# Optimization experiments

Hardware: AMD Instinct MI355X
Metric: run time of the kernel (lower is better)

## Reference

```python
import jax, jax.numpy as jnp
import numpy as np

B, C, H, W, NH = 8, 256, 32, 32, 4  # batch, channels, height, width, heads


def groupnorm(x, w, b, eps=1e-5):
    # GroupNorm with 1 group: normalize over (C,H,W) per sample
    mu = x.mean(axis=(1, 2, 3), keepdims=True)
    var = x.var(axis=(1, 2, 3), keepdims=True)
    xn = (x - mu) * jax.lax.rsqrt(var + eps)
    return xn * w[None, :, None, None] + b[None, :, None, None]


def setup_inputs() -> dict:
    key = jax.random.key(0)
    ks = jax.random.split(key, 6)
    C4 = 4 * C
    s = lambda k, shape, scale: jax.random.normal(k, shape, jnp.float32) * scale
    return {
        "x": jax.random.normal(ks[0], (B, C, H, W), jnp.float32),
        "qkv_w": s(ks[1], (3 * C, C), 0.05),   # 1x1 conv, no bias
        "uh_w": s(ks[2], (C, C), 0.05),
        "uh_b": jnp.zeros((C,), jnp.float32),
        "n1_w": jnp.ones((C,), jnp.float32),
        "n1_b": jnp.zeros((C,), jnp.float32),
        "n2_w": jnp.ones((C,), jnp.float32),
        "n2_b": jnp.zeros((C,), jnp.float32),
        "f1_w": s(ks[3], (C4, C), 0.05),
        "f1_b": jnp.zeros((C4,), jnp.float32),
        "f2_w": s(ks[4], (C, C4), 0.05),
        "f2_b": jnp.zeros((C,), jnp.float32),
        # torch inits these to 0; use nonzero values so both branches contribute
        "gamma_attn": jnp.array(0.5, jnp.float32),
        "gamma_ffn": jnp.array(0.5, jnp.float32),
    }


def reference(x, qkv_w, uh_w, uh_b, n1_w, n1_b, n2_w, n2_b,
              f1_w, f1_b, f2_w, f2_b, gamma_attn, gamma_ffn):
    Bx, Cx, Hx, Wx = x.shape
    N = Hx * Wx
    dk = Cx // NH
    # --- attention branch (eval mode: DropPath is identity) ---
    xn = groupnorm(x, n1_w, n1_b).reshape(Bx, Cx, N)
    qkv = jnp.einsum('oc,bcn->bon', qkv_w, xn)          # 1x1 conv == channel matmul
    q, k, v = [t.reshape(Bx, NH, dk, N) for t in jnp.split(qkv, 3, axis=1)]
    scores = jnp.einsum('bhdi,bhdj->bhij', q, k) / np.float32(np.sqrt(dk))
    attn = jax.nn.softmax(scores, axis=-1)               # [B,H,N,N]
    out = jnp.einsum('bhij,bhdj->bhdi', attn, v).reshape(Bx, Cx, N)
    uh = jnp.einsum('oc,bcn->bon', uh_w, out) + uh_b[None, :, None]
    x2 = x + gamma_attn * uh.reshape(Bx, Cx, Hx, Wx)
    # --- FFN branch ---
    h = groupnorm(x2, n2_w, n2_b).reshape(Bx, Cx, N)
    h = jax.nn.silu(jnp.einsum('oc,bcn->bon', f1_w, h) + f1_b[None, :, None])
    h = jnp.einsum('oc,bcn->bon', f2_w, h) + f2_b[None, :, None]
    return x2 + gamma_ffn * h.reshape(Bx, Cx, Hx, Wx)
```

## Files before the change

kernel.cpp:

```cpp
#include <hip/hip_runtime.h>
#include <math.h>

#define Bsz 8
#define Cch 256
#define Nsp 1024
#define NHd 4
#define QS  0.18033688011112042f

using bf16x8  = __attribute__((ext_vector_type(8))) short;
using f32x4   = __attribute__((ext_vector_type(4))) float;
using ushort8 = __attribute__((ext_vector_type(8))) unsigned short;
#define MFMA(a,b,c) __builtin_amdgcn_mfma_f32_16x16x32_bf16(a,b,c,0,0,0)

__device__ inline unsigned short f2bf(float f) {
    unsigned int u = __float_as_uint(f);
    u = u + 0x7fffu + ((u >> 16) & 1u);
    return (unsigned short)(u >> 16);
}
__device__ inline float bf2f(unsigned short u) {
    return __uint_as_float((unsigned int)u << 16);
}
__device__ inline unsigned int cvtpk(float lo, float hi) {
    unsigned int r;
    asm("v_cvt_pk_bf16_f32 %0, %1, %2" : "=v"(r) : "v"(lo), "v"(hi));
    return r;
}

__global__ __launch_bounds__(256) void wconv_gn(const float* __restrict__ a, const float* __restrict__ b,
                                                const float* __restrict__ c, const float* __restrict__ d,
                                                unsigned short* __restrict__ o,
                                                const float* __restrict__ x,
                                                float* __restrict__ part) {
    if (blockIdx.x < 3072) {
        size_t i = (size_t)blockIdx.x * 256 + threadIdx.x;
        float v;
        if (i < 196608) v = a[i];
        else if (i < 262144) v = b[i - 196608];
        else if (i < 524288) v = c[i - 262144];
        else v = d[i - 524288];
        o[i] = f2bf(v);
        return;
    }
    int blk = blockIdx.x - 3072;
    int bb = blk >> 6;
    const float* xb = x + (size_t)bb * (Cch * Nsp) + (size_t)(blk & 63) * 4096;
    int t = threadIdx.x;
    float s = 0.f, s2 = 0.f;
    for (int i = t; i < 4096; i += 256) { float v = xb[i]; s += v; s2 += v * v; }
    __shared__ float sh[256], sh2[256];
    sh[t] = s; sh2[t] = s2; __syncthreads();
    for (int off = 128; off; off >>= 1) {
        if (t < off) { sh[t] += sh[t + off]; sh2[t] += sh2[t + off]; }
        __syncthreads();
    }
    if (t == 0) { part[blk * 2] = sh[0]; part[blk * 2 + 1] = sh2[0]; }
}

__global__ __launch_bounds__(256) void gn_apply_t(const float* __restrict__ x,
                                                  const float* __restrict__ part, int npart,
                                                  const float* __restrict__ w,
                                                  const float* __restrict__ bb,
                                                  unsigned short* __restrict__ out_cl) {
    int b = blockIdx.z, c0 = blockIdx.y * 64, n0 = blockIdx.x * 64;
    __shared__ float tile[64][65];
    __shared__ float smu, srs;
    int t = threadIdx.x;
    if (t < 64) {
        float s = 0.f, s2 = 0.f;
        for (int u = t; u < npart; u += 64) {
            s += part[(b * npart + u) * 2]; s2 += part[(b * npart + u) * 2 + 1];
        }
        for (int m = 1; m < 64; m <<= 1) { s += __shfl_xor(s, m); s2 += __shfl_xor(s2, m); }
        if (t == 0) {
            float inv_n = 1.f / (Cch * Nsp);
            float mu = s * inv_n;
            float var = s2 * inv_n - mu * mu;
            smu = mu; srs = rsqrtf(var + 1e-5f);
        }
    }
    const float* xb = x + ((size_t)b * Cch + c0) * Nsp + n0;
    for (int i = 0; i < 16; i++) {
        int e = t + i * 256; int r = e >> 6, c = e & 63;
        tile[r][c] = xb[(size_t)r * Nsp + c];
    }
    __syncthreads();
    float mu = smu, rs = srs;
    unsigned short* ob = out_cl + ((size_t)b * Nsp + n0) * Cch + c0;
    for (int i = 0; i < 16; i++) {
        int e = t + i * 256; int nr = e >> 6, nc = e & 63;
        int c = c0 + nc;
        float v = (tile[nc][nr] - mu) * rs * w[c] + bb[c];
        ob[(size_t)nr * Cch + nc] = f2bf(v);
    }
}

template<int K, int KL, int NFRAG>
__global__ __launch_bounds__(256, (K > 256) ? 2 : 4) void gemm_lds(
        const unsigned short* __restrict__ W,
        const unsigned short* __restrict__ Xcl,
        int epi, int act, int xmode,
        unsigned short* __restrict__ ocl, int Ocl, int ocol0,
        unsigned short* __restrict__ orm,
        float* __restrict__ pf, const float* __restrict__ res,
        unsigned short* __restrict__ x2cl,
        const float* __restrict__ gamma, const float* __restrict__ bias,
        float* __restrict__ part,
        const float* __restrict__ gnpart,
        const float* __restrict__ gnw, const float* __restrict__ gnb) {
    static_assert(KL == 256, "K-loop hardcoded for KL=256 (8 steps)");
    constexpr int NK = K / KL;
    constexpr int NTILE = NFRAG * 16;
    constexpr int CPR = KL / 8;
    constexpr int TOTCH = NTILE * CPR;
    int b = blockIdx.z, nb = blockIdx.x, ob = blockIdx.y;
    int t = threadIdx.x, w = t >> 6, l = t & 63, lg = l >> 4, lm = l & 15;
    __shared__ unsigned short Xs[(NK > 1 ? 2 : 1) * NTILE * KL];
    __shared__ float sgn[2];
    unsigned short* Xs0 = Xs;
    unsigned short* Xs1 = Xs + (NK > 1 ? NTILE * KL : 0);
    const unsigned short* Xb = Xcl + ((size_t)b * Nsp + nb * NTILE) * K;
    int o_base = ob * 256 + w * 64;
    const unsigned short* Wp = W + (size_t)(o_base + lm) * K + 8 * lg;
    int m8 = lm & 7;

    bf16x8 wr[3][4];
    #define WLOAD(sl, g_) do {                                             \
        const unsigned short* wp_ = Wp + ((g_) >> 3) * KL + ((g_) & 7) * 32; \
        wr[sl][0] = *(const bf16x8*)(wp_);                                 \
        wr[sl][1] = *(const bf16x8*)(wp_ + (size_t)16 * K);                \
        wr[sl][2] = *(const bf16x8*)(wp_ + (size_t)32 * K);                \
        wr[sl][3] = *(const bf16x8*)(wp_ + (size_t)48 * K);                \
    } while (0)
    WLOAD(0, 0);
    WLOAD(1, 1);

    if (xmode == 0) {
        #pragma unroll
        for (int i = 0; i < TOTCH / 256; i++) {
            int c = i * 256 + t;
            int n = c / CPR, s = c % CPR;
            int gc = s ^ (n & 7);
            *(bf16x8*)&Xs0[c * 8] = *(const bf16x8*)(Xb + (size_t)n * K + gc * 8);
        }
    } else if (xmode == 1) {
        if (t < 64) {
            float s = gnpart[(b * 64 + t) * 2], s2 = gnpart[(b * 64 + t) * 2 + 1];
            for (int m = 1; m < 64; m <<= 1) { s += __shfl_xor(s, m); s2 += __shfl_xor(s2, m); }
            if (t == 0) {
                float inv_n = 1.f / (Cch * Nsp);
                float mu = s * inv_n;
                float var = s2 * inv_n - mu * mu;
                sgn[0] = mu; sgn[1] = rsqrtf(var + 1e-5f);
            }
        }
        __syncthreads();
        float mu = sgn[0], rs = sgn[1];
        #pragma unroll
        for (int i = 0; i < TOTCH / 256; i++) {
            int c = i * 256 + t;
            int n = c / CPR, s = c % CPR;
            int gc = s ^ (n & 7);
            ushort8 xv = *(const ushort8*)(Xb + (size_t)n * K + gc * 8);
            f32x4 w0 = *(const f32x4*)(gnw + gc * 8);
            f32x4 w1 = *(const f32x4*)(gnw + gc * 8 + 4);
            f32x4 b0 = *(const f32x4*)(gnb + gc * 8);
            f32x4 b1 = *(const f32x4*)(gnb + gc * 8 + 4);
            ushort8 rr;
            #pragma unroll
            for (int j = 0; j < 4; j++) {
                rr[j]     = f2bf((bf2f(xv[j])     - mu) * rs * w0[j] + b0[j]);
                rr[4 + j] = f2bf((bf2f(xv[4 + j]) - mu) * rs * w1[j] + b1[j]);
            }
            *(ushort8*)&Xs0[c * 8] = rr;
        }
    } else {
        const size_t SPO = (size_t)Bsz * Nsp * Cch;
        #pragma unroll
        for (int i = 0; i < TOTCH / 256; i++) {
            int c = i * 256 + t;
            int n = c / CPR, s = c % CPR;
            int gc = s ^ (n & 7);
            const unsigned short* p0 = Xb + (size_t)n * K + gc * 8;
            int h = gc >> 3;
            int gn = nb * NTILE + n;
            float a0[8] = {};
            float lsum = 0.f;
            #pragma unroll
            for (int sp = 0; sp < 4; sp++) {
                ushort8 ov = *(const ushort8*)(p0 + (size_t)sp * SPO);
                #pragma unroll
                for (int j = 0; j < 8; j++) a0[j] += bf2f(ov[j]);
                lsum += gnpart[(((size_t)sp * Bsz + b) * NHd + h) * Nsp + gn];
            }
            float inv = 1.f / lsum;
            ushort8 rr;
            #pragma unroll
            for (int j = 0; j < 8; j++) rr[j] = f2bf(a0[j] * inv);
            *(ushort8*)&Xs0[c * 8] = rr;
        }
    }
    __syncthreads();

    f32x4 acc[4][NFRAG] = {};
    bf16x8 st[TOTCH / 256];
    #define KSTEP(sl, s_, Xp) do {                                         \
        _Pragma("unroll")                                                  \
        for (int nf = 0; nf < NFRAG; nf++) {                               \
            int slot = ((s_) * 4 + lg) ^ m8;                               \
            bf16x8 xf = *(const bf16x8*)&(Xp)[((nf * 16 + lm) * CPR + slot) * 8]; \
            acc[0][nf] = MFMA(wr[sl][0], xf, acc[0][nf]);                  \
            acc[1][nf] = MFMA(wr[sl][1], xf, acc[1][nf]);                  \
            acc[2][nf] = MFMA(wr[sl][2], xf, acc[2][nf]);                  \
            acc[3][nf] = MFMA(wr[sl][3], xf, acc[3][nf]);                  \
        }                                                                  \
    } while (0)

    #pragma unroll
    for (int g = 0; g < 8 * NK; g++) {
        const int r = g >> 3, s = g & 7;
        if (NK > 1 && r + 1 < NK && s == 0) {
            #pragma unroll
            for (int i = 0; i < TOTCH / 256; i++) {
                int c = i * 256 + t;
                int n = c / CPR, sc = c % CPR;
                int gc = sc ^ (n & 7);
                st[i] = *(const bf16x8*)(Xb + (size_t)n * K + (r + 1) * KL + gc * 8);
            }
        }
        if (g + 2 < 8 * NK) WLOAD((g + 2) % 3, g + 2);
        {
            const unsigned short* Xp = (r & 1) ? Xs1 : Xs0;
            KSTEP(g % 3, s, Xp);
        }
        if (NK > 1 && r + 1 < NK && s == 6) {
            unsigned short* dst = (r & 1) ? Xs0 : Xs1;
            #pragma unroll
            for (int i = 0; i < TOTCH / 256; i++) {
                int c = i * 256 + t;
                *(bf16x8*)&dst[c * 8] = st[i];
            }
        }
        if (NK > 1 && r + 1 < NK && s == 7) __syncthreads();
    }
    #undef WLOAD
    #undef KSTEP

    if (epi == 0) {
        if (act == 3 && o_base >= 512) {
            #pragma unroll
            for (int nf = 0; nf < NFRAG; nf++) {
                int n = nb * NTILE + nf * 16 + lm;
                #pragma unroll
                for (int q = 0; q < 4; q++)
                    #pragma unroll
                    for (int r = 0; r < 4; r++) {
                        int o = o_base + q * 16 + 4 * lg + r - 512;
                        orm[((size_t)b * Cch + o) * Nsp + n] = f2bf(acc[q][nf][r]);
                    }
            }
        } else {
            float sc = (act == 3 && o_base < 256) ? QS : 1.f;
            #pragma unroll
            for (int nf = 0; nf < NFRAG; nf++) {
                int n = nb * NTILE + nf * 16 + lm;
                unsigned short* dst = ocl + ((size_t)b * Nsp + n) * Ocl + ocol0 + o_base + 4 * lg;
                #pragma unroll
                for (int q = 0; q < 4; q++) {
                    unsigned long long pk = 0;
                    #pragma unroll
                    for (int r = 0; r < 4; r++) {
                        int o = o_base + q * 16 + 4 * lg + r;
                        float v = acc[q][nf][r];
                        if (bias) v += bias[o];
                        if (act == 1) v = v / (1.f + __expf(-v));
                        else v *= sc;
                        pk |= (unsigned long long)f2bf(v) << (16 * r);
                    }
                    *(unsigned long long*)(dst + q * 16) = pk;
                }
            }
        }
    } else if (epi == 2) {
        float g = gamma[0];
        float ps = 0.f, ps2 = 0.f;
        #pragma unroll
        for (int nf = 0; nf < NFRAG; nf++) {
            int n = nb * NTILE + nf * 16 + lm;
            unsigned short* cdst = x2cl + ((size_t)b * Nsp + n) * Cch + o_base + 4 * lg;
            #pragma unroll
            for (int q = 0; q < 4; q++) {
                unsigned long long pk = 0;
                #pragma unroll
                for (int r = 0; r < 4; r++) {
                    int o = o_base + q * 16 + 4 * lg + r;
                    float v = acc[q][nf][r];
                    if (bias) v += bias[o];
                    size_t idx = ((size_t)b * Cch + o) * Nsp + n;
                    float ov = res[idx] + g * v;
                    pf[idx] = ov;
                    ps += ov; ps2 += ov * ov;
                    pk |= (unsigned long long)f2bf(ov) << (16 * r);
                }
                *(unsigned long long*)(cdst + q * 16) = pk;
            }
        }
        float* rsh  = (float*)&Xs[0];
        float* rsh2 = rsh + 256;
        __syncthreads();
        rsh[t] = ps; rsh2[t] = ps2; __syncthreads();
        for (int off = 128; off; off >>= 1) {
            if (t < off) { rsh[t] += rsh[t + off]; rsh2[t] += rsh2[t + off]; }
            __syncthreads();
        }
        if (t == 0) {
            int slot = b * gridDim.x + nb;
            part[slot * 2] = rsh[0]; part[slot * 2 + 1] = rsh2[0];
        }
    } else {
        float g = gamma[0];
        #pragma unroll
        for (int nf = 0; nf < NFRAG; nf++) {
            int n = nb * NTILE + nf * 16 + lm;
            #pragma unroll
            for (int q = 0; q < 4; q++) {
                #pragma unroll
                for (int r = 0; r < 4; r++) {
                    int o = o_base + q * 16 + 4 * lg + r;
                    size_t idx = ((size_t)b * Cch + o) * Nsp + n;
                    pf[idx] = res[idx] + g * (acc[q][nf][r] + bias[o]);
                }
            }
        }
    }
}

__global__ __launch_bounds__(256) void attn_mfma8(const unsigned short* __restrict__ qk,
                                                  const unsigned short* __restrict__ v,
                                                  unsigned short* __restrict__ Opart,
                                                  float* __restrict__ lpart) {
    int L = blockIdx.x;
    int xcd = L & 7, jj = L >> 3;
    int g = xcd * 4 + (jj >> 5);
    int m = jj & 31;
    int h = g & 3, b = g >> 2;
    int ib = m & 7, sp = m >> 3;
    int t = threadIdx.x, w = t >> 6, l = t & 63, lg = l >> 4, lm = l & 15;
    __shared__ unsigned short KVs[2][4096];
    __shared__ unsigned short P[4][2][32][36];
    int i0 = ib * 128 + w * 32;
    int j0 = sp * 256;
    const unsigned short* qb = qk + ((size_t)b * Nsp + i0 + lm) * 512 + h * 64 + 8 * lg;
    bf16x8 qf00 = *(const bf16x8*)(qb);
    bf16x8 qf01 = *(const bf16x8*)(qb + 32);
    bf16x8 qf10 = *(const bf16x8*)(qb + 16 * 512);
    bf16x8 qf11 = *(const bf16x8*)(qb + 16 * 512 + 32);

    const unsigned short *gs0, *gs1;
    int lo0, lo1;
    size_t gstep;
    if (t < 128) {
        int c = 2 * t;
        int r = c >> 3, s = c & 7, swr = r & 7;
        const unsigned short* rowp = qk + ((size_t)b * Nsp + j0 + r) * 512 + 256 + h * 64;
        gs0 = rowp + ((s ^ swr) * 8);
        gs1 = rowp + (((s + 1) ^ swr) * 8);
        lo0 = c * 8; lo1 = lo0 + 8;
        gstep = (size_t)32 * 512;
    } else {
        int c = 2 * (t - 128);
        int d = c >> 2, s = c & 3, swd = d & 3;
        const unsigned short* rowp = v + ((size_t)b * Cch + h * 64 + d) * Nsp + j0;
        gs0 = rowp + ((s ^ swd) * 8);
        gs1 = rowp + (((s + 1) ^ swd) * 8);
        lo0 = 2048 + c * 8; lo1 = lo0 + 8;
        gstep = 32;
    }
    int cA = (lg ^ (lm & 7)) * 8;
    int cB = ((4 + lg) ^ (lm & 7)) * 8;
    int cV = (lg ^ (lm & 3)) * 8;

    f32x4 O00 = {}, O01 = {}, O02 = {}, O03 = {};
    f32x4 O10 = {}, O11 = {}, O12 = {}, O13 = {};
    float ls0 = 0.f, ls1 = 0.f;
    bf16x8 sg0, sg1;

    #define ISSUE(tile) do { sg0 = *(const bf16x8*)(gs0 + (size_t)(tile) * gstep); \
                             sg1 = *(const bf16x8*)(gs1 + (size_t)(tile) * gstep); } while (0)
    #define WRITE(bu) do { *(bf16x8*)&KVs[bu][lo0] = sg0; \
                           *(bf16x8*)&KVs[bu][lo1] = sg1; } while (0)
    #define QKC8(bu, pb) do {                                                     \
        const unsigned short* Ka = KVs[bu] + lm * 64;                             \
        const unsigned short* Kc = KVs[bu] + (16 + lm) * 64;                      \
        bf16x8 k00 = *(const bf16x8*)(Ka + cA);                                   \
        bf16x8 k01 = *(const bf16x8*)(Ka + cB);                                   \
        bf16x8 k10 = *(const bf16x8*)(Kc + cA);                                   \
        bf16x8 k11 = *(const bf16x8*)(Kc + cB);                                   \
        f32x4 s00 = {}, s01 = {}, s10 = {}, s11 = {};                             \
        s00 = MFMA(k00, qf00, s00); s00 = MFMA(k01, qf01, s00);                   \
        s01 = MFMA(k00, qf10, s01); s01 = MFMA(k01, qf11, s01);                   \
        s10 = MFMA(k10, qf00, s10); s10 = MFMA(k11, qf01, s10);                   \
        s11 = MFMA(k10, qf10, s11); s11 = MFMA(k11, qf11, s11);                   \
        float p0, p1, p2, p3; uint2 pk;                                           \
        p0 = exp2f(s00[0]); p1 = exp2f(s00[1]); p2 = exp2f(s00[2]); p3 = exp2f(s00[3]); \
        ls0 += (p0 + p1) + (p2 + p3);                                             \
        pk.x = cvtpk(p0, p1); pk.y = cvtpk(p2, p3);                               \
        *(uint2*)&P[w][pb][lm][4 * lg] = pk;                                      \
        p0 = exp2f(s01[0]); p1 = exp2f(s01[1]); p2 = exp2f(s01[2]); p3 = exp2f(s01[3]); \
        ls1 += (p0 + p1) + (p2 + p3);                                             \
        pk.x = cvtpk(p0, p1); pk.y = cvtpk(p2, p3);                               \
        *(uint2*)&P[w][pb][16 + lm][4 * lg] = pk;                                 \
        p0 = exp2f(s10[0]); p1 = exp2f(s10[1]); p2 = exp2f(s10[2]); p3 = exp2f(s10[3]); \
        ls0 += (p0 + p1) + (p2 + p3);                                             \
        pk.x = cvtpk(p0, p1); pk.y = cvtpk(p2, p3);                               \
        *(uint2*)&P[w][pb][lm][16 + 4 * lg] = pk;                                 \
        p0 = exp2f(s11[0]); p1 = exp2f(s11[1]); p2 = exp2f(s11[2]); p3 = exp2f(s11[3]); \
        ls1 += (p0 + p1) + (p2 + p3);                                             \
        pk.x = cvtpk(p0, p1); pk.y = cvtpk(p2, p3);                               \
        *(uint2*)&P[w][pb][16 + lm][16 + 4 * lg] = pk;                            \
    } while (0)
    #define PVC8(bu, pb) do {                                                     \
        bf16x8 pa0 = *(const bf16x8*)&P[w][pb][lm][8 * lg];                       \
        bf16x8 pa1 = *(const bf16x8*)&P[w][pb][16 + lm][8 * lg];                  \
        const unsigned short* Vl = KVs[bu] + 2048;                                \
        bf16x8 v0 = *(const bf16x8*)(Vl + lm * 32 + cV);                          \
        bf16x8 v1 = *(const bf16x8*)(Vl + (16 + lm) * 32 + cV);                   \
        bf16x8 v2 = *(const bf16x8*)(Vl + (32 + lm) * 32 + cV);                   \
        bf16x8 v3 = *(const bf16x8*)(Vl + (48 + lm) * 32 + cV);                   \
        O00 = MFMA(v0, pa0, O00); O10 = MFMA(v0, pa1, O10);                       \
        O01 = MFMA(v1, pa0, O01); O11 = MFMA(v1, pa1, O11);                       \
        O02 = MFMA(v2, pa0, O02); O12 = MFMA(v2, pa1, O12);                       \
        O03 = MFMA(v3, pa0, O03); O13 = MFMA(v3, pa1, O13);                       \
    } while (0)

    ISSUE(0); WRITE(0); __syncthreads();
    ISSUE(1);
    QKC8(0, 0);
    __syncthreads();
    WRITE(1);
    __syncthreads();
    #pragma unroll
    for (int tt = 1; tt < 8; tt++) {
        if (tt < 7) ISSUE(tt + 1);
        QKC8(tt & 1, tt & 1);
        PVC8((tt - 1) & 1, (tt - 1) & 1);
        __syncthreads();
        if (tt < 7) WRITE((tt + 1) & 1);
        __syncthreads();
    }
    PVC8(1, 1);
    #undef ISSUE
    #undef WRITE
    #undef QKC8
    #undef PVC8

    ls0 += __shfl_xor(ls0, 16); ls0 += __shfl_xor(ls0, 32);
    ls1 += __shfl_xor(ls1, 16); ls1 += __shfl_xor(ls1, 32);
    if (lg == 0) {
        float* lp = lpart + (((size_t)sp * Bsz + b) * NHd + h) * Nsp + i0 + lm;
        lp[0] = ls0;
        lp[16] = ls1;
    }
    unsigned short* ob0 = Opart + (((size_t)sp * Bsz + b) * Nsp + i0 + lm) * Cch + h * 64 + 4 * lg;
    unsigned short* ob1 = ob0 + (size_t)16 * Cch;
    uint2 pk;
    #define STO(dt, Oa, Ob_) \
        pk.x = cvtpk(Oa[0], Oa[1]); pk.y = cvtpk(Oa[2], Oa[3]); \
        *(uint2*)(ob0 + dt * 16) = pk; \
        pk.x = cvtpk(Ob_[0], Ob_[1]); pk.y = cvtpk(Ob_[2], Ob_[3]); \
        *(uint2*)(ob1 + dt * 16) = pk;
    STO(0, O00, O10) STO(1, O01, O11) STO(2, O02, O12) STO(3, O03, O13)
    #undef STO
}

extern "C" void kernel_launch(void* const* d_in, const int* in_sizes, int n_in,
                              void* d_out, int out_size, void* d_ws, size_t ws_size,
                              hipStream_t stream) {
    const float* x      = (const float*)d_in[0];
    const float* qkv_w  = (const float*)d_in[1];
    const float* uh_w   = (const float*)d_in[2];
    const float* uh_b   = (const float*)d_in[3];
    const float* n1_w   = (const float*)d_in[4];
    const float* n1_b   = (const float*)d_in[5];
    const float* n2_w   = (const float*)d_in[6];
    const float* n2_b   = (const float*)d_in[7];
    const float* f1_w   = (const float*)d_in[8];
    const float* f1_b   = (const float*)d_in[9];
    const float* f2_w   = (const float*)d_in[10];
    const float* f2_b   = (const float*)d_in[11];
    const float* g_attn = (const float*)d_in[12];
    const float* g_ffn  = (const float*)d_in[13];
    float* out = (float*)d_out;
    char* ws = (char*)d_ws;

    float*          part1   = (float*)(ws + 1024);
    float*          part2   = (float*)(ws + 5120);
    unsigned short* wbf     = (unsigned short*)(ws + 16384);
    unsigned short* xn_cl   = (unsigned short*)(ws + 2097152);
    float*          lpart   = (float*)(ws + 2097152);
    unsigned short* qk_cl   = (unsigned short*)(ws + 6291456);
    unsigned short* vbuf    = (unsigned short*)(ws + 14680064);
    unsigned short* x2cl    = (unsigned short*)(ws + 14680064);
    unsigned short* Opart   = (unsigned short*)(ws + 23068672);
    unsigned short* h1_cl   = (unsigned short*)(ws + 31457280);
    float*          x2      = (float*)(ws + 50331648);

    unsigned short* wbf_qkv = wbf;
    unsigned short* wbf_uh  = wbf + 196608;
    unsigned short* wbf_f1  = wbf + 262144;
    unsigned short* wbf_f2  = wbf + 524288;

    wconv_gn<<<3584, 256, 0, stream>>>(qkv_w, uh_w, f1_w, f2_w, wbf, x, part1);

    gn_apply_t<<<dim3(16, 4, Bsz), 256, 0, stream>>>(x, part1, 64, n1_w, n1_b, xn_cl);
    gemm_lds<256, 256, 2><<<dim3(32, 3, Bsz), 256, 0, stream>>>(wbf_qkv, xn_cl, 0, 3, 0,
        qk_cl, 512, 0, vbuf, nullptr, nullptr, nullptr, nullptr, nullptr, nullptr,
        nullptr, nullptr, nullptr);
    attn_mfma8<<<1024, 256, 0, stream>>>(qk_cl, vbuf, Opart, lpart);
    gemm_lds<256, 256, 1><<<dim3(64, 1, Bsz), 256, 0, stream>>>(wbf_uh, Opart, 2, 0, 2,
        nullptr, 0, 0, nullptr, x2, x, x2cl, g_attn, uh_b, part2,
        lpart, nullptr, nullptr);

    gemm_lds<256, 256, 2><<<dim3(32, 4, Bsz), 256, 0, stream>>>(wbf_f1, x2cl, 0, 1, 1,
        h1_cl, 1024, 0, nullptr, nullptr, nullptr, nullptr, nullptr, f1_b, nullptr,
        part2, n2_w, n2_b);
    gemm_lds<1024, 256, 2><<<dim3(32, 1, Bsz), 256, 0, stream>>>(wbf_f2, h1_cl, 5, 0, 0,
        nullptr, 0, 0, nullptr, out, x2, nullptr, g_ffn, f2_b, nullptr,
        nullptr, nullptr, nullptr);
}
```

Before: 118.4 us.

## Fuse GroupNorm-1 into QKV GEMM and fuse both FFN GEMMs into one kernel

Drops the separate gn_apply_t transpose kernel. The QKV GEMM now reads fp32 x directly, normalizes it and stores it channel-last into LDS (new xmode 3). The FFN1 and FFN2 GEMMs are merged into a single ffn_fused kernel that keeps the 32x1024 SiLU hidden tile in LDS, so the h1 round trip through global memory and two launches are removed. The trade-off is 80KB of LDS per block in ffn_fused, which limits occupancy, and only 256 blocks for that stage. The generic GEMM drops its multi-round K path.

```diff
diff --git a/kernel.cpp b/kernel.cpp
--- a/kernel.cpp
+++ b/kernel.cpp
@@ -56,46 +56,8 @@
     if (t == 0) { part[blk * 2] = sh[0]; part[blk * 2 + 1] = sh2[0]; }
 }
 
-__global__ __launch_bounds__(256) void gn_apply_t(const float* __restrict__ x,
-                                                  const float* __restrict__ part, int npart,
-                                                  const float* __restrict__ w,
-                                                  const float* __restrict__ bb,
-                                                  unsigned short* __restrict__ out_cl) {
-    int b = blockIdx.z, c0 = blockIdx.y * 64, n0 = blockIdx.x * 64;
-    __shared__ float tile[64][65];
-    __shared__ float smu, srs;
-    int t = threadIdx.x;
-    if (t < 64) {
-        float s = 0.f, s2 = 0.f;
-        for (int u = t; u < npart; u += 64) {
-            s += part[(b * npart + u) * 2]; s2 += part[(b * npart + u) * 2 + 1];
-        }
-        for (int m = 1; m < 64; m <<= 1) { s += __shfl_xor(s, m); s2 += __shfl_xor(s2, m); }
-        if (t == 0) {
-            float inv_n = 1.f / (Cch * Nsp);
-            float mu = s * inv_n;
-            float var = s2 * inv_n - mu * mu;
-            smu = mu; srs = rsqrtf(var + 1e-5f);
-        }
-    }
-    const float* xb = x + ((size_t)b * Cch + c0) * Nsp + n0;
-    for (int i = 0; i < 16; i++) {
-        int e = t + i * 256; int r = e >> 6, c = e & 63;
-        tile[r][c] = xb[(size_t)r * Nsp + c];
-    }
-    __syncthreads();
-    float mu = smu, rs = srs;
-    unsigned short* ob = out_cl + ((size_t)b * Nsp + n0) * Cch + c0;
-    for (int i = 0; i < 16; i++) {
-        int e = t + i * 256; int nr = e >> 6, nc = e & 63;
-        int c = c0 + nc;
-        float v = (tile[nc][nr] - mu) * rs * w[c] + bb[c];
-        ob[(size_t)nr * Cch + nc] = f2bf(v);
-    }
-}
-
 template<int K, int KL, int NFRAG>
-__global__ __launch_bounds__(256, (K > 256) ? 2 : 4) void gemm_lds(
+__global__ __launch_bounds__(256, 4) void gemm_lds(
         const unsigned short* __restrict__ W,
         const unsigned short* __restrict__ Xcl,
         int epi, int act, int xmode,
@@ -107,25 +69,22 @@
         float* __restrict__ part,
         const float* __restrict__ gnpart,
         const float* __restrict__ gnw, const float* __restrict__ gnb) {
-    static_assert(KL == 256, "K-loop hardcoded for KL=256 (8 steps)");
-    constexpr int NK = K / KL;
+    static_assert(KL == 256 && K == 256, "single-round K only");
     constexpr int NTILE = NFRAG * 16;
     constexpr int CPR = KL / 8;
     constexpr int TOTCH = NTILE * CPR;
     int b = blockIdx.z, nb = blockIdx.x, ob = blockIdx.y;
     int t = threadIdx.x, w = t >> 6, l = t & 63, lg = l >> 4, lm = l & 15;
-    __shared__ unsigned short Xs[(NK > 1 ? 2 : 1) * NTILE * KL];
+    __shared__ unsigned short Xs[NTILE * KL];
     __shared__ float sgn[2];
-    unsigned short* Xs0 = Xs;
-    unsigned short* Xs1 = Xs + (NK > 1 ? NTILE * KL : 0);
     const unsigned short* Xb = Xcl + ((size_t)b * Nsp + nb * NTILE) * K;
     int o_base = ob * 256 + w * 64;
     const unsigned short* Wp = W + (size_t)(o_base + lm) * K + 8 * lg;
-    int m8 = lm & 7;
+    int m8 = lm & 15 & 7;
 
     bf16x8 wr[3][4];
     #define WLOAD(sl, g_) do {                                             \
-        const unsigned short* wp_ = Wp + ((g_) >> 3) * KL + ((g_) & 7) * 32; \
+        const unsigned short* wp_ = Wp + ((g_) & 7) * 32;                  \
         wr[sl][0] = *(const bf16x8*)(wp_);                                 \
         wr[sl][1] = *(const bf16x8*)(wp_ + (size_t)16 * K);                \
         wr[sl][2] = *(const bf16x8*)(wp_ + (size_t)32 * K);                \
@@ -140,7 +99,7 @@
             int c = i * 256 + t;
             int n = c / CPR, s = c % CPR;
             int gc = s ^ (n & 7);
-            *(bf16x8*)&Xs0[c * 8] = *(const bf16x8*)(Xb + (size_t)n * K + gc * 8);
+            *(bf16x8*)&Xs[c * 8] = *(const bf16x8*)(Xb + (size_t)n * K + gc * 8);
         }
     } else if (xmode == 1) {
         if (t < 64) {
@@ -171,9 +130,9 @@
                 rr[j]     = f2bf((bf2f(xv[j])     - mu) * rs * w0[j] + b0[j]);
                 rr[4 + j] = f2bf((bf2f(xv[4 + j]) - mu) * rs * w1[j] + b1[j]);
             }
-            *(ushort8*)&Xs0[c * 8] = rr;
-        }
-    } else {
+            *(ushort8*)&Xs[c * 8] = rr;
+        }
+    } else if (xmode == 2) {
         const size_t SPO = (size_t)Bsz * Nsp * Cch;
         #pragma unroll
         for (int i = 0; i < TOTCH / 256; i++) {
@@ -196,51 +155,54 @@
             ushort8 rr;
             #pragma unroll
             for (int j = 0; j < 8; j++) rr[j] = f2bf(a0[j] * inv);
-            *(ushort8*)&Xs0[c * 8] = rr;
+            *(ushort8*)&Xs[c * 8] = rr;
+        }
+    } else {
+        if (t < 64) {
+            float s = gnpart[(b * 64 + t) * 2], s2 = gnpart[(b * 64 + t) * 2 + 1];
+            for (int m = 1; m < 64; m <<= 1) { s += __shfl_xor(s, m); s2 += __shfl_xor(s2, m); }
+            if (t == 0) {
+                float inv_n = 1.f / (Cch * Nsp);
+                float mu = s * inv_n;
+                float var = s2 * inv_n - mu * mu;
+                sgn[0] = mu; sgn[1] = rsqrtf(var + 1e-5f);
+            }
+        }
+        __syncthreads();
+        float mu = sgn[0], rs = sgn[1];
+        int n = t & 31;
+        #pragma unroll
+        for (int i = 0; i < 4; i++) {
+            int G = i * 8 + (t >> 5);
+            const float* xr = res + ((size_t)b * Cch + G * 8) * Nsp + (size_t)nb * NTILE + n;
+            ushort8 rr;
+            #pragma unroll
+            for (int j = 0; j < 8; j++) {
+                float val = xr[(size_t)j * Nsp];
+                rr[j] = f2bf((val - mu) * rs * gnw[G * 8 + j] + gnb[G * 8 + j]);
+            }
+            int slot = G ^ (n & 7);
+            *(ushort8*)&Xs[(n * 32 + slot) * 8] = rr;
         }
     }
     __syncthreads();
 
     f32x4 acc[4][NFRAG] = {};
-    bf16x8 st[TOTCH / 256];
-    #define KSTEP(sl, s_, Xp) do {                                         \
+    #define KSTEP(sl, s_) do {                                             \
         _Pragma("unroll")                                                  \
         for (int nf = 0; nf < NFRAG; nf++) {                               \
             int slot = ((s_) * 4 + lg) ^ m8;                               \
-            bf16x8 xf = *(const bf16x8*)&(Xp)[((nf * 16 + lm) * CPR + slot) * 8]; \
+            bf16x8 xf = *(const bf16x8*)&Xs[((nf * 16 + lm) * CPR + slot) * 8]; \
             acc[0][nf] = MFMA(wr[sl][0], xf, acc[0][nf]);                  \
             acc[1][nf] = MFMA(wr[sl][1], xf, acc[1][nf]);                  \
             acc[2][nf] = MFMA(wr[sl][2], xf, acc[2][nf]);                  \
             acc[3][nf] = MFMA(wr[sl][3], xf, acc[3][nf]);                  \
         }                                                                  \
     } while (0)
-
     #pragma unroll
-    for (int g = 0; g < 8 * NK; g++) {
-        const int r = g >> 3, s = g & 7;
-        if (NK > 1 && r + 1 < NK && s == 0) {
-            #pragma unroll
-            for (int i = 0; i < TOTCH / 256; i++) {
-                int c = i * 256 + t;
-                int n = c / CPR, sc = c % CPR;
-                int gc = sc ^ (n & 7);
-                st[i] = *(const bf16x8*)(Xb + (size_t)n * K + (r + 1) * KL + gc * 8);
-            }
-        }
-        if (g + 2 < 8 * NK) WLOAD((g + 2) % 3, g + 2);
-        {
-            const unsigned short* Xp = (r & 1) ? Xs1 : Xs0;
-            KSTEP(g % 3, s, Xp);
-        }
-        if (NK > 1 && r + 1 < NK && s == 6) {
-            unsigned short* dst = (r & 1) ? Xs0 : Xs1;
-            #pragma unroll
-            for (int i = 0; i < TOTCH / 256; i++) {
-                int c = i * 256 + t;
-                *(bf16x8*)&dst[c * 8] = st[i];
-            }
-        }
-        if (NK > 1 && r + 1 < NK && s == 7) __syncthreads();
+    for (int s = 0; s < 8; s++) {
+        if (s < 6) WLOAD((s + 2) % 3, s + 2);
+        KSTEP(s % 3, s);
     }
     #undef WLOAD
     #undef KSTEP
@@ -280,7 +242,7 @@
                 }
             }
         }
-    } else if (epi == 2) {
+    } else {
         float g = gamma[0];
         float ps = 0.f, ps2 = 0.f;
         #pragma unroll
@@ -316,19 +278,150 @@
             int slot = b * gridDim.x + nb;
             part[slot * 2] = rsh[0]; part[slot * 2 + 1] = rsh2[0];
         }
-    } else {
-        float g = gamma[0];
-        #pragma unroll
-        for (int nf = 0; nf < NFRAG; nf++) {
-            int n = nb * NTILE + nf * 16 + lm;
-            #pragma unroll
-            for (int q = 0; q < 4; q++) {
-                #pragma unroll
-                for (int r = 0; r < 4; r++) {
-                    int o = o_base + q * 16 + 4 * lg + r;
-                    size_t idx = ((size_t)b * Cch + o) * Nsp + n;
-                    pf[idx] = res[idx] + g * (acc[q][nf][r] + bias[o]);
-                }
+    }
+}
+
+__global__ __launch_bounds__(256, 2) void ffn_fused(
+        const unsigned short* __restrict__ Wf1,
+        const unsigned short* __restrict__ Wf2,
+        const unsigned short* __restrict__ x2cl,
+        const float* __restrict__ gnpart,
+        const float* __restrict__ gnw, const float* __restrict__ gnb,
+        const float* __restrict__ f1b, const float* __restrict__ f2b,
+        const float* __restrict__ gamma,
+        const float* __restrict__ x2, float* __restrict__ out) {
+    int b = blockIdx.z, nb = blockIdx.x;
+    int t = threadIdx.x, w = t >> 6, l = t & 63, lg = l >> 4, lm = l & 15;
+    __shared__ unsigned short Xs[32 * 256];
+    __shared__ unsigned short H[4][32 * 256];
+    __shared__ float sgn[2];
+    const unsigned short* Xb = x2cl + ((size_t)b * Nsp + nb * 32) * 256;
+    int m8 = lm & 7;
+
+    bf16x8 wr[3][4];
+    const unsigned short* Wp;
+    #define WLOADF(sl, g_, KK) do {                                        \
+        const unsigned short* wp_ = Wp + ((g_) >> 3) * 256 + ((g_) & 7) * 32; \
+        wr[sl][0] = *(const bf16x8*)(wp_);                                 \
+        wr[sl][1] = *(const bf16x8*)(wp_ + (size_t)16 * (KK));             \
+        wr[sl][2] = *(const bf16x8*)(wp_ + (size_t)32 * (KK));             \
+        wr[sl][3] = *(const bf16x8*)(wp_ + (size_t)48 * (KK));             \
+    } while (0)
+
+    if (t < 64) {
+        float s = gnpart[(b * 64 + t) * 2], s2 = gnpart[(b * 64 + t) * 2 + 1];
+        for (int m = 1; m < 64; m <<= 1) { s += __shfl_xor(s, m); s2 += __shfl_xor(s2, m); }
+        if (t == 0) {
+            float inv_n = 1.f / (Cch * Nsp);
+            float mu = s * inv_n;
+            float var = s2 * inv_n - mu * mu;
+            sgn[0] = mu; sgn[1] = rsqrtf(var + 1e-5f);
+        }
+    }
+    Wp = Wf1 + (size_t)(w * 64 + lm) * 256 + 8 * lg;
+    WLOADF(0, 0, 256);
+    WLOADF(1, 1, 256);
+    __syncthreads();
+    {
+        float mu = sgn[0], rs = sgn[1];
+        #pragma unroll
+        for (int i = 0; i < 4; i++) {
+            int c = i * 256 + t;
+            int n = c / 32, s = c % 32;
+            int gc = s ^ (n & 7);
+            ushort8 xv = *(const ushort8*)(Xb + (size_t)n * 256 + gc * 8);
+            f32x4 w0 = *(const f32x4*)(gnw + gc * 8);
+            f32x4 w1 = *(const f32x4*)(gnw + gc * 8 + 4);
+            f32x4 b0 = *(const f32x4*)(gnb + gc * 8);
+            f32x4 b1 = *(const f32x4*)(gnb + gc * 8 + 4);
+            ushort8 rr;
+            #pragma unroll
+            for (int j = 0; j < 4; j++) {
+                rr[j]     = f2bf((bf2f(xv[j])     - mu) * rs * w0[j] + b0[j]);
+                rr[4 + j] = f2bf((bf2f(xv[4 + j]) - mu) * rs * w1[j] + b1[j]);
+            }
+            *(ushort8*)&Xs[c * 8] = rr;
+        }
+    }
+    __syncthreads();
+
+    f32x4 acc[4][2];
+    #define KSTEPF(sl, s_, Xp) do {                                        \
+        _Pragma("unroll")                                                  \
+        for (int nf = 0; nf < 2; nf++) {                                   \
+            int slot = ((s_) * 4 + lg) ^ m8;                               \
+            bf16x8 xf = *(const bf16x8*)&(Xp)[((nf * 16 + lm) * 32 + slot) * 8]; \
+            acc[0][nf] = MFMA(wr[sl][0], xf, acc[0][nf]);                  \
+            acc[1][nf] = MFMA(wr[sl][1], xf, acc[1][nf]);                  \
+            acc[2][nf] = MFMA(wr[sl][2], xf, acc[2][nf]);                  \
+            acc[3][nf] = MFMA(wr[sl][3], xf, acc[3][nf]);                  \
+        }                                                                  \
+    } while (0)
+    #define F1PASS(obp, NEXTPROLOG) do {                                   \
+        _Pragma("unroll")                                                  \
+        for (int q = 0; q < 4; q++)                                        \
+            _Pragma("unroll")                                              \
+            for (int nf = 0; nf < 2; nf++) acc[q][nf] = (f32x4){0.f, 0.f, 0.f, 0.f}; \
+        _Pragma("unroll")                                                  \
+        for (int s = 0; s < 8; s++) {                                      \
+            if (s < 6) WLOADF((s + 2) % 3, s + 2, 256);                    \
+            KSTEPF(s % 3, s, Xs);                                          \
+        }                                                                  \
+        NEXTPROLOG;                                                        \
+        _Pragma("unroll")                                                  \
+        for (int nf = 0; nf < 2; nf++) {                                   \
+            int n = nf * 16 + lm;                                          \
+            _Pragma("unroll")                                              \
+            for (int q = 0; q < 4; q++) {                                  \
+                unsigned long long pk = 0;                                 \
+                _Pragma("unroll")                                          \
+                for (int r = 0; r < 4; r++) {                              \
+                    int oin = w * 64 + q * 16 + 4 * lg + r;                \
+                    float v = acc[q][nf][r] + f1b[(obp) * 256 + oin];      \
+                    v = v / (1.f + __expf(-v));                            \
+                    pk |= (unsigned long long)f2bf(v) << (16 * r);         \
+                }                                                          \
+                int G = w * 8 + q * 2 + (lg >> 1);                         \
+                int slot = G ^ (n & 7);                                    \
+                *(unsigned long long*)&H[obp][(n * 32 + slot) * 8 + 4 * (lg & 1)] = pk; \
+            }                                                              \
+        }                                                                  \
+    } while (0)
+
+    F1PASS(0, { Wp = Wf1 + (size_t)(256 + w * 64 + lm) * 256 + 8 * lg;
+                WLOADF(0, 0, 256); WLOADF(1, 1, 256); });
+    F1PASS(1, { Wp = Wf1 + (size_t)(512 + w * 64 + lm) * 256 + 8 * lg;
+                WLOADF(0, 0, 256); WLOADF(1, 1, 256); });
+    F1PASS(2, { Wp = Wf1 + (size_t)(768 + w * 64 + lm) * 256 + 8 * lg;
+                WLOADF(0, 0, 256); WLOADF(1, 1, 256); });
+    F1PASS(3, { Wp = Wf2 + (size_t)(w * 64 + lm) * 1024 + 8 * lg;
+                WLOADF(0, 0, 1024); WLOADF(1, 1, 1024); });
+    __syncthreads();
+
+    #pragma unroll
+    for (int q = 0; q < 4; q++)
+        #pragma unroll
+        for (int nf = 0; nf < 2; nf++) acc[q][nf] = (f32x4){0.f, 0.f, 0.f, 0.f};
+    #pragma unroll
+    for (int g = 0; g < 32; g++) {
+        if (g < 30) WLOADF((g + 2) % 3, g + 2, 1024);
+        KSTEPF(g % 3, g & 7, H[g >> 3]);
+    }
+    #undef WLOADF
+    #undef KSTEPF
+    #undef F1PASS
+
+    float gm = gamma[0];
+    #pragma unroll
+    for (int nf = 0; nf < 2; nf++) {
+        int n = nb * 32 + nf * 16 + lm;
+        #pragma unroll
+        for (int q = 0; q < 4; q++) {
+            #pragma unroll
+            for (int r = 0; r < 4; r++) {
+                int o = w * 64 + q * 16 + 4 * lg + r;
+                size_t idx = ((size_t)b * Cch + o) * Nsp + n;
+                out[idx] = x2[idx] + gm * (acc[q][nf][r] + f2b[o]);
             }
         }
     }
@@ -495,13 +588,11 @@
     float*          part1   = (float*)(ws + 1024);
     float*          part2   = (float*)(ws + 5120);
     unsigned short* wbf     = (unsigned short*)(ws + 16384);
-    unsigned short* xn_cl   = (unsigned short*)(ws + 2097152);
     float*          lpart   = (float*)(ws + 2097152);
     unsigned short* qk_cl   = (unsigned short*)(ws + 6291456);
     unsigned short* vbuf    = (unsigned short*)(ws + 14680064);
     unsigned short* x2cl    = (unsigned short*)(ws + 14680064);
     unsigned short* Opart   = (unsigned short*)(ws + 23068672);
-    unsigned short* h1_cl   = (unsigned short*)(ws + 31457280);
     float*          x2      = (float*)(ws + 50331648);
 
     unsigned short* wbf_qkv = wbf;
@@ -511,19 +602,15 @@
 
     wconv_gn<<<3584, 256, 0, stream>>>(qkv_w, uh_w, f1_w, f2_w, wbf, x, part1);
 
-    gn_apply_t<<<dim3(16, 4, Bsz), 256, 0, stream>>>(x, part1, 64, n1_w, n1_b, xn_cl);
-    gemm_lds<256, 256, 2><<<dim3(32, 3, Bsz), 256, 0, stream>>>(wbf_qkv, xn_cl, 0, 3, 0,
-        qk_cl, 512, 0, vbuf, nullptr, nullptr, nullptr, nullptr, nullptr, nullptr,
-        nullptr, nullptr, nullptr);
+    gemm_lds<256, 256, 2><<<dim3(32, 3, Bsz), 256, 0, stream>>>(wbf_qkv,
+        (const unsigned short*)x, 0, 3, 3,
+        qk_cl, 512, 0, vbuf, nullptr, x, nullptr, nullptr, nullptr, nullptr,
+        part1, n1_w, n1_b);
     attn_mfma8<<<1024, 256, 0, stream>>>(qk_cl, vbuf, Opart, lpart);
     gemm_lds<256, 256, 1><<<dim3(64, 1, Bsz), 256, 0, stream>>>(wbf_uh, Opart, 2, 0, 2,
         nullptr, 0, 0, nullptr, x2, x, x2cl, g_attn, uh_b, part2,
         lpart, nullptr, nullptr);
 
-    gemm_lds<256, 256, 2><<<dim3(32, 4, Bsz), 256, 0, stream>>>(wbf_f1, x2cl, 0, 1, 1,
-        h1_cl, 1024, 0, nullptr, nullptr, nullptr, nullptr, nullptr, f1_b, nullptr,
-        part2, n2_w, n2_b);
-    gemm_lds<1024, 256, 2><<<dim3(32, 1, Bsz), 256, 0, stream>>>(wbf_f2, h1_cl, 5, 0, 0,
-        nullptr, 0, 0, nullptr, out, x2, nullptr, g_ffn, f2_b, nullptr,
-        nullptr, nullptr, nullptr);
-}
+    ffn_fused<<<dim3(32, 1, Bsz), 256, 0, stream>>>(wbf_f1, wbf_f2, x2cl,
+        part2, n2_w, n2_b, f1_b, f2_b, g_ffn, x2, out);
+}
```

Measured after the change: 113.4 us. 1.04x faster.

## Fuse GroupNorm1 apply into QKV GEMM and add dedicated 8-wave F2 GEMM

Applied to the files above, without the earlier changes.

Removes the separate gn_apply_t kernel. The QKV GEMM now reads fp32 x directly in channel-major order, normalizes it, converts to bf16 and transposes it into the swizzled LDS tile (new xmode 3). This saves a launch and the round trip of the xn_cl intermediate through memory. The K=1024 F2 projection moves to its own 512-thread kernel in which each wave covers 32 output channels, with a deeper weight register pipeline and a double-buffered LDS X tile. The generic GEMM is simplified to a single K round at occupancy 4. The fused load uses strided fp32 global reads, which may be less coalesced than the old transpose kernel.

```diff
diff --git a/kernel.cpp b/kernel.cpp
--- a/kernel.cpp
+++ b/kernel.cpp
@@ -56,46 +56,8 @@
     if (t == 0) { part[blk * 2] = sh[0]; part[blk * 2 + 1] = sh2[0]; }
 }
 
-__global__ __launch_bounds__(256) void gn_apply_t(const float* __restrict__ x,
-                                                  const float* __restrict__ part, int npart,
-                                                  const float* __restrict__ w,
-                                                  const float* __restrict__ bb,
-                                                  unsigned short* __restrict__ out_cl) {
-    int b = blockIdx.z, c0 = blockIdx.y * 64, n0 = blockIdx.x * 64;
-    __shared__ float tile[64][65];
-    __shared__ float smu, srs;
-    int t = threadIdx.x;
-    if (t < 64) {
-        float s = 0.f, s2 = 0.f;
-        for (int u = t; u < npart; u += 64) {
-            s += part[(b * npart + u) * 2]; s2 += part[(b * npart + u) * 2 + 1];
-        }
-        for (int m = 1; m < 64; m <<= 1) { s += __shfl_xor(s, m); s2 += __shfl_xor(s2, m); }
-        if (t == 0) {
-            float inv_n = 1.f / (Cch * Nsp);
-            float mu = s * inv_n;
-            float var = s2 * inv_n - mu * mu;
-            smu = mu; srs = rsqrtf(var + 1e-5f);
-        }
-    }
-    const float* xb = x + ((size_t)b * Cch + c0) * Nsp + n0;
-    for (int i = 0; i < 16; i++) {
-        int e = t + i * 256; int r = e >> 6, c = e & 63;
-        tile[r][c] = xb[(size_t)r * Nsp + c];
-    }
-    __syncthreads();
-    float mu = smu, rs = srs;
-    unsigned short* ob = out_cl + ((size_t)b * Nsp + n0) * Cch + c0;
-    for (int i = 0; i < 16; i++) {
-        int e = t + i * 256; int nr = e >> 6, nc = e & 63;
-        int c = c0 + nc;
-        float v = (tile[nc][nr] - mu) * rs * w[c] + bb[c];
-        ob[(size_t)nr * Cch + nc] = f2bf(v);
-    }
-}
-
 template<int K, int KL, int NFRAG>
-__global__ __launch_bounds__(256, (K > 256) ? 2 : 4) void gemm_lds(
+__global__ __launch_bounds__(256, 4) void gemm_lds(
         const unsigned short* __restrict__ W,
         const unsigned short* __restrict__ Xcl,
         int epi, int act, int xmode,
@@ -107,17 +69,14 @@
         float* __restrict__ part,
         const float* __restrict__ gnpart,
         const float* __restrict__ gnw, const float* __restrict__ gnb) {
-    static_assert(KL == 256, "K-loop hardcoded for KL=256 (8 steps)");
-    constexpr int NK = K / KL;
+    static_assert(KL == 256 && K == 256, "single-round K only");
     constexpr int NTILE = NFRAG * 16;
     constexpr int CPR = KL / 8;
     constexpr int TOTCH = NTILE * CPR;
     int b = blockIdx.z, nb = blockIdx.x, ob = blockIdx.y;
     int t = threadIdx.x, w = t >> 6, l = t & 63, lg = l >> 4, lm = l & 15;
-    __shared__ unsigned short Xs[(NK > 1 ? 2 : 1) * NTILE * KL];
+    __shared__ unsigned short Xs[NTILE * KL];
     __shared__ float sgn[2];
-    unsigned short* Xs0 = Xs;
-    unsigned short* Xs1 = Xs + (NK > 1 ? NTILE * KL : 0);
     const unsigned short* Xb = Xcl + ((size_t)b * Nsp + nb * NTILE) * K;
     int o_base = ob * 256 + w * 64;
     const unsigned short* Wp = W + (size_t)(o_base + lm) * K + 8 * lg;
@@ -125,7 +84,7 @@
 
     bf16x8 wr[3][4];
     #define WLOAD(sl, g_) do {                                             \
-        const unsigned short* wp_ = Wp + ((g_) >> 3) * KL + ((g_) & 7) * 32; \
+        const unsigned short* wp_ = Wp + ((g_) & 7) * 32;                  \
         wr[sl][0] = *(const bf16x8*)(wp_);                                 \
         wr[sl][1] = *(const bf16x8*)(wp_ + (size_t)16 * K);                \
         wr[sl][2] = *(const bf16x8*)(wp_ + (size_t)32 * K);                \
@@ -140,7 +99,7 @@
             int c = i * 256 + t;
             int n = c / CPR, s = c % CPR;
             int gc = s ^ (n & 7);
-            *(bf16x8*)&Xs0[c * 8] = *(const bf16x8*)(Xb + (size_t)n * K + gc * 8);
+            *(bf16x8*)&Xs[c * 8] = *(const bf16x8*)(Xb + (size_t)n * K + gc * 8);
         }
     } else if (xmode == 1) {
         if (t < 64) {
@@ -171,9 +130,9 @@
                 rr[j]     = f2bf((bf2f(xv[j])     - mu) * rs * w0[j] + b0[j]);
                 rr[4 + j] = f2bf((bf2f(xv[4 + j]) - mu) * rs * w1[j] + b1[j]);
             }
-            *(ushort8*)&Xs0[c * 8] = rr;
-        }
-    } else {
+            *(ushort8*)&Xs[c * 8] = rr;
+        }
+    } else if (xmode == 2) {
         const size_t SPO = (size_t)Bsz * Nsp * Cch;
         #pragma unroll
         for (int i = 0; i < TOTCH / 256; i++) {
@@ -196,51 +155,54 @@
             ushort8 rr;
             #pragma unroll
             for (int j = 0; j < 8; j++) rr[j] = f2bf(a0[j] * inv);
-            *(ushort8*)&Xs0[c * 8] = rr;
+            *(ushort8*)&Xs[c * 8] = rr;
+        }
+    } else {
+        if (t < 64) {
+            float s = gnpart[(b * 64 + t) * 2], s2 = gnpart[(b * 64 + t) * 2 + 1];
+            for (int m = 1; m < 64; m <<= 1) { s += __shfl_xor(s, m); s2 += __shfl_xor(s2, m); }
+            if (t == 0) {
+                float inv_n = 1.f / (Cch * Nsp);
+                float mu = s * inv_n;
+                float var = s2 * inv_n - mu * mu;
+                sgn[0] = mu; sgn[1] = rsqrtf(var + 1e-5f);
+            }
+        }
+        __syncthreads();
+        float mu = sgn[0], rs = sgn[1];
+        int n = t & 31;
+        #pragma unroll
+        for (int i = 0; i < 4; i++) {
+            int G = i * 8 + (t >> 5);
+            const float* xr = res + ((size_t)b * Cch + G * 8) * Nsp + (size_t)nb * NTILE + n;
+            ushort8 rr;
+            #pragma unroll
+            for (int j = 0; j < 8; j++) {
+                float val = xr[(size_t)j * Nsp];
+                rr[j] = f2bf((val - mu) * rs * gnw[G * 8 + j] + gnb[G * 8 + j]);
+            }
+            int slot = G ^ (n & 7);
+            *(ushort8*)&Xs[(n * 32 + slot) * 8] = rr;
         }
     }
     __syncthreads();
 
     f32x4 acc[4][NFRAG] = {};
-    bf16x8 st[TOTCH / 256];
-    #define KSTEP(sl, s_, Xp) do {                                         \
+    #define KSTEP(sl, s_) do {                                             \
         _Pragma("unroll")                                                  \
         for (int nf = 0; nf < NFRAG; nf++) {                               \
             int slot = ((s_) * 4 + lg) ^ m8;                               \
-            bf16x8 xf = *(const bf16x8*)&(Xp)[((nf * 16 + lm) * CPR + slot) * 8]; \
+            bf16x8 xf = *(const bf16x8*)&Xs[((nf * 16 + lm) * CPR + slot) * 8]; \
             acc[0][nf] = MFMA(wr[sl][0], xf, acc[0][nf]);                  \
             acc[1][nf] = MFMA(wr[sl][1], xf, acc[1][nf]);                  \
             acc[2][nf] = MFMA(wr[sl][2], xf, acc[2][nf]);                  \
             acc[3][nf] = MFMA(wr[sl][3], xf, acc[3][nf]);                  \
         }                                                                  \
     } while (0)
-
     #pragma unroll
-    for (int g = 0; g < 8 * NK; g++) {
-        const int r = g >> 3, s = g & 7;
-        if (NK > 1 && r + 1 < NK && s == 0) {
-            #pragma unroll
-            for (int i = 0; i < TOTCH / 256; i++) {
-                int c = i * 256 + t;
-                int n = c / CPR, sc = c % CPR;
-                int gc = sc ^ (n & 7);
-                st[i] = *(const bf16x8*)(Xb + (size_t)n * K + (r + 1) * KL + gc * 8);
-            }
-        }
-        if (g + 2 < 8 * NK) WLOAD((g + 2) % 3, g + 2);
-        {
-            const unsigned short* Xp = (r & 1) ? Xs1 : Xs0;
-            KSTEP(g % 3, s, Xp);
-        }
-        if (NK > 1 && r + 1 < NK && s == 6) {
-            unsigned short* dst = (r & 1) ? Xs0 : Xs1;
-            #pragma unroll
-            for (int i = 0; i < TOTCH / 256; i++) {
-                int c = i * 256 + t;
-                *(bf16x8*)&dst[c * 8] = st[i];
-            }
-        }
-        if (NK > 1 && r + 1 < NK && s == 7) __syncthreads();
+    for (int s = 0; s < 8; s++) {
+        if (s < 6) WLOAD((s + 2) % 3, s + 2);
+        KSTEP(s % 3, s);
     }
     #undef WLOAD
     #undef KSTEP
@@ -280,7 +242,7 @@
                 }
             }
         }
-    } else if (epi == 2) {
+    } else {
         float g = gamma[0];
         float ps = 0.f, ps2 = 0.f;
         #pragma unroll
@@ -316,19 +278,88 @@
             int slot = b * gridDim.x + nb;
             part[slot * 2] = rsh[0]; part[slot * 2 + 1] = rsh2[0];
         }
-    } else {
-        float g = gamma[0];
+    }
+}
+
+__global__ __launch_bounds__(512, 2) void f2_gemm(
+        const unsigned short* __restrict__ Wf2,
+        const unsigned short* __restrict__ h1,
+        const float* __restrict__ f2b,
+        const float* __restrict__ gamma,
+        const float* __restrict__ x2,
+        float* __restrict__ out) {
+    int b = blockIdx.z, nb = blockIdx.x;
+    int t = threadIdx.x, w = t >> 6, l = t & 63, lg = l >> 4, lm = l & 15;
+    __shared__ unsigned short Xs[2][32 * 256];
+    const unsigned short* Xb = h1 + ((size_t)b * Nsp + nb * 32) * 1024;
+    int m8 = lm & 7;
+    const unsigned short* Wp = Wf2 + (size_t)(w * 32 + lm) * 1024 + 8 * lg;
+
+    bf16x8 wr[5][2];
+    #define WL2(sl, g_) do {                                    \
+        const unsigned short* wp_ = Wp + (g_) * 32;             \
+        wr[sl][0] = *(const bf16x8*)(wp_);                      \
+        wr[sl][1] = *(const bf16x8*)(wp_ + (size_t)16 * 1024);  \
+    } while (0)
+    WL2(0, 0); WL2(1, 1); WL2(2, 2); WL2(3, 3);
+
+    #pragma unroll
+    for (int i = 0; i < 2; i++) {
+        int c = i * 512 + t;
+        int n = c >> 5, s = c & 31;
+        int gc = s ^ (n & 7);
+        *(bf16x8*)&Xs[0][c * 8] = *(const bf16x8*)(Xb + (size_t)n * 1024 + gc * 8);
+    }
+    __syncthreads();
+
+    f32x4 acc[2][2] = {};
+    bf16x8 st[2];
+    #pragma unroll
+    for (int g = 0; g < 32; g++) {
+        const int r = g >> 3, s = g & 7;
+        if (r < 3 && s == 0) {
+            #pragma unroll
+            for (int i = 0; i < 2; i++) {
+                int c = i * 512 + t;
+                int n = c >> 5, sc = c & 31;
+                int gc = sc ^ (n & 7);
+                st[i] = *(const bf16x8*)(Xb + (size_t)n * 1024 + (r + 1) * 256 + gc * 8);
+            }
+        }
+        if (g + 4 < 32) WL2((g + 4) % 5, g + 4);
+        {
+            const unsigned short* Xp = Xs[r & 1];
+            int slot = (s * 4 + lg) ^ m8;
+            #pragma unroll
+            for (int nf = 0; nf < 2; nf++) {
+                bf16x8 xf = *(const bf16x8*)&Xp[((nf * 16 + lm) * 32 + slot) * 8];
+                acc[0][nf] = MFMA(wr[g % 5][0], xf, acc[0][nf]);
+                acc[1][nf] = MFMA(wr[g % 5][1], xf, acc[1][nf]);
+            }
+        }
+        if (r < 3 && s == 6) {
+            unsigned short* dst = Xs[(r & 1) ^ 1];
+            #pragma unroll
+            for (int i = 0; i < 2; i++) {
+                int c = i * 512 + t;
+                *(bf16x8*)&dst[c * 8] = st[i];
+            }
+        }
+        if (r < 3 && s == 7) __syncthreads();
+    }
+    #undef WL2
+
+    float gm = gamma[0];
+    #pragma unroll
+    for (int nf = 0; nf < 2; nf++) {
+        int n = nb * 32 + nf * 16 + lm;
         #pragma unroll
-        for (int nf = 0; nf < NFRAG; nf++) {
-            int n = nb * NTILE + nf * 16 + lm;
-            #pragma unroll
-            for (int q = 0; q < 4; q++) {
-                #pragma unroll
-                for (int r = 0; r < 4; r++) {
-                    int o = o_base + q * 16 + 4 * lg + r;
-                    size_t idx = ((size_t)b * Cch + o) * Nsp + n;
-                    pf[idx] = res[idx] + g * (acc[q][nf][r] + bias[o]);
-                }
+        for (int ch = 0; ch < 2; ch++) {
+            #pragma unroll
+            for (int rr = 0; rr < 4; rr++) {
+                int o = w * 32 + ch * 16 + 4 * lg + rr;
+                size_t idx = ((size_t)b * Cch + o) * Nsp + n;
+                out[idx] = x2[idx] + gm * (acc[ch][nf][rr] + f2b[o]);
             }
         }
     }
@@ -495,7 +526,6 @@
     float*          part1   = (float*)(ws + 1024);
     float*          part2   = (float*)(ws + 5120);
     unsigned short* wbf     = (unsigned short*)(ws + 16384);
-    unsigned short* xn_cl   = (unsigned short*)(ws + 2097152);
     float*          lpart   = (float*)(ws + 2097152);
     unsigned short* qk_cl   = (unsigned short*)(ws + 6291456);
     unsigned short* vbuf    = (unsigned short*)(ws + 14680064);
@@ -511,10 +541,10 @@
 
     wconv_gn<<<3584, 256, 0, stream>>>(qkv_w, uh_w, f1_w, f2_w, wbf, x, part1);
 
-    gn_apply_t<<<dim3(16, 4, Bsz), 256, 0, stream>>>(x, part1, 64, n1_w, n1_b, xn_cl);
-    gemm_lds<256, 256, 2><<<dim3(32, 3, Bsz), 256, 0, stream>>>(wbf_qkv, xn_cl, 0, 3, 0,
-        qk_cl, 512, 0, vbuf, nullptr, nullptr, nullptr, nullptr, nullptr, nullptr,
-        nullptr, nullptr, nullptr);
+    gemm_lds<256, 256, 2><<<dim3(32, 3, Bsz), 256, 0, stream>>>(wbf_qkv,
+        (const unsigned short*)x, 0, 3, 3,
+        qk_cl, 512, 0, vbuf, nullptr, x, nullptr, nullptr, nullptr, nullptr,
+        part1, n1_w, n1_b);
     attn_mfma8<<<1024, 256, 0, stream>>>(qk_cl, vbuf, Opart, lpart);
     gemm_lds<256, 256, 1><<<dim3(64, 1, Bsz), 256, 0, stream>>>(wbf_uh, Opart, 2, 0, 2,
         nullptr, 0, 0, nullptr, x2, x, x2cl, g_attn, uh_b, part2,
@@ -523,7 +553,5 @@
     gemm_lds<256, 256, 2><<<dim3(32, 4, Bsz), 256, 0, stream>>>(wbf_f1, x2cl, 0, 1, 1,
         h1_cl, 1024, 0, nullptr, nullptr, nullptr, nullptr, nullptr, f1_b, nullptr,
         part2, n2_w, n2_b);
-    gemm_lds<1024, 256, 2><<<dim3(32, 1, Bsz), 256, 0, stream>>>(wbf_f2, h1_cl, 5, 0, 0,
-        nullptr, 0, 0, nullptr, out, x2, nullptr, g_ffn, f2_b, nullptr,
-        nullptr, nullptr, nullptr);
-}
+    f2_gemm<<<dim3(32, 1, Bsz), 512, 0, stream>>>(wbf_f2, h1_cl, f2_b, g_ffn, x2, out);
+}
```

After: 116.2 us. Within noise of the previous version (-1.9%).
